# Performance work log

Measured on AMD Instinct MI355X. Metric: run time of the kernel, lower is better.

The kernel has to match this reference:

```python
import jax, jax.numpy as jnp
import numpy as np
import math

DIM = 2048
N_HEADS = 32
N_KV_HEADS = 8
HEAD_DIM = DIM // N_HEADS  # 64
N_REP = N_HEADS // N_KV_HEADS  # 4
BATCH = 1
SEQ = 2048


def rope_cos_sin(seq_len, head_dim, dtype=jnp.float32):
    inv_freq = 1.0 / (10000.0 ** (jnp.arange(0, head_dim, 2, dtype=jnp.float32) / head_dim))
    t = jnp.arange(seq_len, dtype=jnp.float32)
    freqs = jnp.outer(t, inv_freq)            # [S, D/2]
    emb = jnp.concatenate([freqs, freqs], -1)  # [S, D]
    return jnp.cos(emb).astype(dtype), jnp.sin(emb).astype(dtype)


def rotate_half(x):
    x1 = x[..., ::2]
    x2 = x[..., 1::2]
    return jnp.concatenate([-x2, x1], axis=-1)


def setup_inputs() -> dict:
    key = jax.random.key(0)
    ks = jax.random.split(key, 5)
    scale = 1.0 / math.sqrt(DIM)
    x = jax.random.normal(ks[0], (BATCH, SEQ, DIM), jnp.float32)
    wq = jax.random.normal(ks[1], (DIM, N_HEADS * HEAD_DIM), jnp.float32) * scale
    wk = jax.random.normal(ks[2], (DIM, N_KV_HEADS * HEAD_DIM), jnp.float32) * scale
    wv = jax.random.normal(ks[3], (DIM, N_KV_HEADS * HEAD_DIM), jnp.float32) * scale
    wo = jax.random.normal(ks[4], (N_HEADS * HEAD_DIM, DIM), jnp.float32) * scale
    mask = jnp.tril(jnp.ones((SEQ, SEQ), jnp.int32))[None, None]  # [1,1,S,S]
    return {"x": x, "mask": mask, "wq": wq, "wk": wk, "wv": wv, "wo": wo}


def reference(x, mask, wq, wk, wv, wo):
    B, S, _ = x.shape
    q = (x @ wq).reshape(B, S, N_HEADS, HEAD_DIM).transpose(0, 2, 1, 3)     # [B,H,S,D]
    k = (x @ wk).reshape(B, S, N_KV_HEADS, HEAD_DIM).transpose(0, 2, 1, 3)  # [B,Hkv,S,D]
    v = (x @ wv).reshape(B, S, N_KV_HEADS, HEAD_DIM).transpose(0, 2, 1, 3)
    cos, sin = rope_cos_sin(S, HEAD_DIM)  # [S,D]
    q = q * cos + rotate_half(q) * sin
    k = k * cos + rotate_half(k) * sin
    if N_REP > 1:
        k = jnp.repeat(k, N_REP, axis=1)
        v = jnp.repeat(v, N_REP, axis=1)
    scores = jnp.einsum("bhqd,bhkd->bhqk", q, k) / math.sqrt(HEAD_DIM)
    scores = jnp.where(mask == 0, -jnp.inf, scores)
    attn = jax.nn.softmax(scores, axis=-1)
    out = jnp.einsum("bhqk,bhkd->bhqd", attn, v)  # [B,H,S,D]
    out = out.transpose(0, 2, 1, 3).reshape(B, S, N_HEADS * HEAD_DIM)
    return out @ wo
```

## Files before the change

kernel.cpp:

```cpp
#include <hip/hip_runtime.h>
#include <hip/hip_bf16.h>

#define DIM 2048
#define SEQ 2048
#define NH 32
#define HD 64
#define NKV 8
#define QKV_LD 3072

typedef __attribute__((ext_vector_type(8))) short bf16x8;
typedef __attribute__((ext_vector_type(4))) float f32x4;
typedef unsigned short ushort_t;

__device__ inline unsigned short f2bf(float f) {
    union { float f; unsigned int u; } v; v.f = f;
    unsigned int r = v.u + 0x7fffu + ((v.u >> 16) & 1u);
    return (unsigned short)(r >> 16);
}
__device__ inline float bf2f(ushort_t u) {
    union { unsigned int u; float f; } v; v.u = ((unsigned int)u) << 16; return v.f;
}

__device__ inline void async_cp16(const void* g, void* l) {
    __builtin_amdgcn_global_load_lds(
        (const __attribute__((address_space(1))) unsigned int*)g,
        (__attribute__((address_space(3))) unsigned int*)l, 16, 0, 0);
}
__device__ inline void lgkm_fence() {
    __asm__ volatile("s_waitcnt lgkmcnt(0)" ::: "memory");
}

__global__ __launch_bounds__(256) void convert_kernel(
    const float* __restrict__ X, ushort_t* __restrict__ Xb)
{
    int i = (blockIdx.x * 256 + threadIdx.x) * 4;
    float4 v = *(const float4*)(X + i);
    ushort_t o[4] = { f2bf(v.x), f2bf(v.y), f2bf(v.z), f2bf(v.w) };
    *(uint2*)(Xb + i) = *(uint2*)o;
}

__global__ __launch_bounds__(256) void transpose_kernel(
    const float* __restrict__ W, ushort_t* __restrict__ WT, int N)
{
    __shared__ __align__(16) ushort_t tile[64][72];
    const int n0 = blockIdx.x * 64, k0 = blockIdx.y * 64;
    const int t = threadIdx.x;
    {
        const int tk = t >> 4;
        const int tn = (t & 15) * 4;
        #pragma unroll
        for (int i = 0; i < 4; i++) {
            const int k = tk + i * 16;
            float4 v = *(const float4*)(W + (size_t)(k0 + k) * N + n0 + tn);
            tile[tn + 0][k] = f2bf(v.x);
            tile[tn + 1][k] = f2bf(v.y);
            tile[tn + 2][k] = f2bf(v.z);
            tile[tn + 3][k] = f2bf(v.w);
        }
    }
    __syncthreads();
    {
        const int tn = t >> 2;
        const int tk = (t & 3) * 16;
        uint4 a = *(const uint4*)&tile[tn][tk];
        uint4 b = *(const uint4*)&tile[tn][tk + 8];
        ushort_t* dst = WT + (size_t)(n0 + tn) * DIM + k0 + tk;
        *(uint4*)dst = a;
        *(uint4*)(dst + 8) = b;
    }
}

template<int OUT_F32>
__global__ __launch_bounds__(256) void gemm_kernel(
    const ushort_t* __restrict__ A, const ushort_t* __restrict__ BT,
    void* __restrict__ Cout, int K, int lda, int ldo)
{
    __shared__ __align__(16) ushort_t sA[128 * 32];
    __shared__ __align__(16) ushort_t sB[128 * 32];
    const int tn = blockIdx.x * 128, tm = blockIdx.y * 128;
    const int t = threadIdx.x, wave = t >> 6, lane = t & 63;
    const int m16 = lane & 15, quad = lane >> 4;
    const int wr = (wave >> 1) * 64, wc = (wave & 1) * 64;
    const int srow = lane >> 2;
    const int sce = (lane & 3) * 8;

    f32x4 acc[4][4] = {};

    for (int k0 = 0; k0 < K; k0 += 32) {
        __syncthreads();
        #pragma unroll
        for (int p = 0; p < 2; p++) {
            const int j = wave * 2 + p;
            const int row = j * 16 + srow;
            async_cp16(A  + (size_t)(tm + row) * lda + k0 + sce, &sA[j * 512]);
            async_cp16(BT + (size_t)(tn + row) * K   + k0 + sce, &sB[j * 512]);
        }
        __syncthreads();
        bf16x8 af[4], bf[4];
        #pragma unroll
        for (int mt = 0; mt < 4; mt++)
            af[mt] = *(const bf16x8*)&sA[(wr + mt * 16 + m16) * 32 + quad * 8];
        #pragma unroll
        for (int nt = 0; nt < 4; nt++)
            bf[nt] = *(const bf16x8*)&sB[(wc + nt * 16 + m16) * 32 + quad * 8];
        #pragma unroll
        for (int mt = 0; mt < 4; mt++)
            #pragma unroll
            for (int nt = 0; nt < 4; nt++)
                acc[mt][nt] = __builtin_amdgcn_mfma_f32_16x16x32_bf16(af[mt], bf[nt], acc[mt][nt], 0, 0, 0);
    }

    #pragma unroll
    for (int mt = 0; mt < 4; mt++) {
        const int row = tm + wr + mt * 16 + quad * 4;
        #pragma unroll
        for (int nt = 0; nt < 4; nt++) {
            const int col = tn + wc + nt * 16 + m16;
            #pragma unroll
            for (int r = 0; r < 4; r++) {
                if (OUT_F32)
                    ((float*)Cout)[(size_t)(row + r) * ldo + col] = acc[mt][nt][r];
                else
                    ((ushort_t*)Cout)[(size_t)(row + r) * ldo + col] = f2bf(acc[mt][nt][r]);
            }
        }
    }
}

__global__ __launch_bounds__(256) void rope_kernel(ushort_t* qkv, ushort_t* __restrict__ Kr)
{
    const int gid = blockIdx.x * 256 + threadIdx.x;
    const int lane = gid & 63;
    const int idx = gid >> 6;
    const int s = idx / 40;
    const int hh = idx - s * 40;

    const ushort_t* src;
    ushort_t* dst;
    if (hh < 32) {
        dst = qkv + (size_t)s * QKV_LD + hh * 64;
        src = dst;
    } else {
        src = qkv + (size_t)s * QKV_LD + 2048 + (hh - 32) * 64;
        dst = Kr + ((size_t)(hh - 32) * SEQ + s) * 64;
    }

    const float e = bf2f(src[lane]);
    const int i = lane & 31;
    const float freq = __expf(-(float)i * 0.28782313662425572f);
    const float ang = (float)s * freq;
    const float cv = cosf(ang), sv = sinf(ang);
    const int partner = (lane < 32) ? (2 * lane + 1) : (2 * (lane - 32));
    const float y = __shfl(e, partner, 64);
    const float out = (lane < 32) ? (e * cv - y * sv) : (e * cv + y * sv);
    dst[lane] = f2bf(out);
}

__global__ __launch_bounds__(256) void vtrans_kernel(
    const ushort_t* __restrict__ qkv, ushort_t* __restrict__ Vt)
{
    __shared__ __align__(16) ushort_t tile[64][72];
    const int kvh = blockIdx.x & 7;
    const int s0 = (blockIdx.x >> 3) * 64;
    const int t = threadIdx.x;
    {
        const int sr = t >> 3;
        const int d8 = (t & 7) * 8;
        #pragma unroll
        for (int i = 0; i < 2; i++) {
            const int s = sr + i * 32;
            ushort_t tmp[8];
            *(uint4*)tmp = *(const uint4*)(qkv + (size_t)(s0 + s) * QKV_LD + 2560 + kvh * 64 + d8);
            #pragma unroll
            for (int j = 0; j < 8; j++) tile[d8 + j][s] = tmp[j];
        }
    }
    __syncthreads();
    {
        const int dr = t >> 3;
        const int s8 = (t & 7) * 8;
        #pragma unroll
        for (int i = 0; i < 2; i++) {
            const int d = dr + i * 32;
            *(uint4*)(Vt + ((size_t)kvh * 64 + d) * SEQ + s0 + s8) = *(const uint4*)&tile[d][s8];
        }
    }
}

#define SPS 80
__global__ __launch_bounds__(512, 2) void attn_kernel(
    ushort_t* qkv, const ushort_t* __restrict__ Kr, const ushort_t* __restrict__ Vt)
{
    __shared__ __align__(16) ushort_t sP[8][2][16 * SPS];

    const int t = threadIdx.x, wave = t >> 6, lane = t & 63;
    const int m16 = lane & 15, quad = lane >> 4;
    const int h = blockIdx.x & 31;
    const int p = blockIdx.x >> 5;
    const int grp = wave >> 2;
    const int w4 = wave & 3;
    const int band = grp ? p : 15 - p;
    const int kvh = h >> 2;

    const ushort_t* Krh = Kr + (size_t)kvh * SEQ * 64;
    const ushort_t* Vth = Vt + (size_t)kvh * 64 * SEQ;

    const int nkt = band * 2 + 2;

    int qi[2];
    bf16x8 qf[2][2];
    #pragma unroll
    for (int qa = 0; qa < 2; qa++) {
        qi[qa] = band * 128 + (w4 + qa * 4) * 16 + m16;
        const ushort_t* qp = qkv + (size_t)qi[qa] * QKV_LD + h * 64 + quad * 8;
        qf[qa][0] = *(const bf16x8*)qp;
        qf[qa][1] = *(const bf16x8*)(qp + 32);
    }

    f32x4 oacc[2][4] = {};
    float m_run[2] = { -1e30f, -1e30f };
    float l_run[2] = { 0.f, 0.f };

    bf16x8 kf[4][2];
    #pragma unroll
    for (int knt = 0; knt < 4; knt++) {
        const ushort_t* kp = Krh + (size_t)(knt * 16 + m16) * 64 + quad * 8;
        kf[knt][0] = *(const bf16x8*)kp;
        kf[knt][1] = *(const bf16x8*)(kp + 32);
    }

    for (int kt = 0; kt < nkt; kt++) {
        const int kbase = kt * 64;
        const bool last = (kt == nkt - 1);

        f32x4 sc[2][4] = {};
        #pragma unroll
        for (int qa = 0; qa < 2; qa++) {
            if (qa == 0 && last) continue;
            #pragma unroll
            for (int knt = 0; knt < 4; knt++) {
                sc[qa][knt] = __builtin_amdgcn_mfma_f32_16x16x32_bf16(kf[knt][0], qf[qa][0], sc[qa][knt], 0, 0, 0);
                sc[qa][knt] = __builtin_amdgcn_mfma_f32_16x16x32_bf16(kf[knt][1], qf[qa][1], sc[qa][knt], 0, 0, 0);
            }
        }

        bf16x8 vf[4][2];
        #pragma unroll
        for (int nt = 0; nt < 4; nt++) {
            const ushort_t* vp = Vth + (size_t)(nt * 16 + m16) * SEQ + kbase + quad * 8;
            vf[nt][0] = *(const bf16x8*)vp;
            vf[nt][1] = *(const bf16x8*)(vp + 32);
        }
        if (!last) {
            #pragma unroll
            for (int knt = 0; knt < 4; knt++) {
                const ushort_t* kp = Krh + (size_t)(kbase + 64 + knt * 16 + m16) * 64 + quad * 8;
                kf[knt][0] = *(const bf16x8*)kp;
                kf[knt][1] = *(const bf16x8*)(kp + 32);
            }
        }

        #pragma unroll
        for (int qa = 0; qa < 2; qa++) {
            if (qa == 0 && last) continue;
            const bool domask = (qa == 0) ? (kt == nkt - 2) : last;

            float s[16];
            #pragma unroll
            for (int knt = 0; knt < 4; knt++)
                #pragma unroll
                for (int r = 0; r < 4; r++) {
                    float v = sc[qa][knt][r] * 0.125f;
                    if (domask && (kbase + knt * 16 + quad * 4 + r > qi[qa])) v = -1e30f;
                    s[knt * 4 + r] = v;
                }

            float x0 = fmaxf(s[0], s[1]),  x1 = fmaxf(s[2], s[3]);
            float x2 = fmaxf(s[4], s[5]),  x3 = fmaxf(s[6], s[7]);
            float x4 = fmaxf(s[8], s[9]),  x5 = fmaxf(s[10], s[11]);
            float x6 = fmaxf(s[12], s[13]), x7 = fmaxf(s[14], s[15]);
            float rmax = fmaxf(fmaxf(fmaxf(x0, x1), fmaxf(x2, x3)),
                               fmaxf(fmaxf(x4, x5), fmaxf(x6, x7)));
            rmax = fmaxf(rmax, __shfl_xor(rmax, 16, 64));
            rmax = fmaxf(rmax, __shfl_xor(rmax, 32, 64));

            const float mnew = fmaxf(m_run[qa], rmax);
            const float alpha = __expf(m_run[qa] - mnew);
            m_run[qa] = mnew;

            #pragma unroll
            for (int i = 0; i < 16; i++) s[i] = __expf(s[i] - mnew);
            float y0 = s[0] + s[1],  y1 = s[2] + s[3];
            float y2 = s[4] + s[5],  y3 = s[6] + s[7];
            float y4 = s[8] + s[9],  y5 = s[10] + s[11];
            float y6 = s[12] + s[13], y7 = s[14] + s[15];
            float ps = ((y0 + y1) + (y2 + y3)) + ((y4 + y5) + (y6 + y7));
            ps += __shfl_xor(ps, 16, 64);
            ps += __shfl_xor(ps, 32, 64);
            l_run[qa] = l_run[qa] * alpha + ps;

            ushort_t* sPw = sP[wave][qa];
            #pragma unroll
            for (int knt = 0; knt < 4; knt++) {
                unsigned int u0 = (unsigned int)f2bf(s[knt * 4 + 0]) | ((unsigned int)f2bf(s[knt * 4 + 1]) << 16);
                unsigned int u1 = (unsigned int)f2bf(s[knt * 4 + 2]) | ((unsigned int)f2bf(s[knt * 4 + 3]) << 16);
                uint2 pk; pk.x = u0; pk.y = u1;
                *(uint2*)&sPw[m16 * SPS + knt * 16 + quad * 4] = pk;
            }
            lgkm_fence();
            bf16x8 pf0 = *(const bf16x8*)&sPw[m16 * SPS + quad * 8];
            bf16x8 pf1 = *(const bf16x8*)&sPw[m16 * SPS + 32 + quad * 8];

            #pragma unroll
            for (int nt = 0; nt < 4; nt++) {
                #pragma unroll
                for (int r = 0; r < 4; r++) oacc[qa][nt][r] *= alpha;
                oacc[qa][nt] = __builtin_amdgcn_mfma_f32_16x16x32_bf16(vf[nt][0], pf0, oacc[qa][nt], 0, 0, 0);
                oacc[qa][nt] = __builtin_amdgcn_mfma_f32_16x16x32_bf16(vf[nt][1], pf1, oacc[qa][nt], 0, 0, 0);
            }
        }
    }

    #pragma unroll
    for (int qa = 0; qa < 2; qa++) {
        const float rl = 1.f / l_run[qa];
        #pragma unroll
        for (int nt = 0; nt < 4; nt++) {
            ushort_t pk[4];
            #pragma unroll
            for (int r = 0; r < 4; r++) pk[r] = f2bf(oacc[qa][nt][r] * rl);
            *(uint2*)&qkv[(size_t)qi[qa] * QKV_LD + h * 64 + nt * 16 + quad * 4] = *(uint2*)pk;
        }
    }
}

extern "C" void kernel_launch(void* const* d_in, const int* in_sizes, int n_in,
                              void* d_out, int out_size, void* d_ws, size_t ws_size,
                              hipStream_t stream)
{
    const float* x  = (const float*)d_in[0];
    const float* wq = (const float*)d_in[2];
    const float* wk = (const float*)d_in[3];
    const float* wv = (const float*)d_in[4];
    const float* wo = (const float*)d_in[5];

    ushort_t* WT  = (ushort_t*)d_ws;
    ushort_t* xb  = WT + (size_t)3072 * 2048;
    ushort_t* woT = xb;
    ushort_t* qkv = xb + (size_t)2048 * 2048;
    ushort_t* Kr  = qkv + (size_t)SEQ * QKV_LD;
    ushort_t* Vt  = Kr + (size_t)NKV * SEQ * HD;

    dim3 blk(256);

    convert_kernel<<<(DIM * SEQ) / 1024, blk, 0, stream>>>(x, xb);
    transpose_kernel<<<dim3(32, 32), blk, 0, stream>>>(wq, WT, 2048);
    transpose_kernel<<<dim3(8, 32),  blk, 0, stream>>>(wk, WT + (size_t)2048 * 2048, 512);
    transpose_kernel<<<dim3(8, 32),  blk, 0, stream>>>(wv, WT + (size_t)2560 * 2048, 512);

    gemm_kernel<0><<<dim3(QKV_LD / 128, SEQ / 128), blk, 0, stream>>>(xb, WT, qkv, DIM, DIM, QKV_LD);

    transpose_kernel<<<dim3(32, 32), blk, 0, stream>>>(wo, woT, 2048);

    rope_kernel<<<(SEQ * 40 * 64) / 256, blk, 0, stream>>>(qkv, Kr);
    vtrans_kernel<<<NKV * (SEQ / 64), blk, 0, stream>>>(qkv, Vt);

    attn_kernel<<<8 * NH, dim3(512), 0, stream>>>(qkv, Kr, Vt);

    gemm_kernel<1><<<dim3(DIM / 128, SEQ / 128), blk, 0, stream>>>(qkv, woT, d_out, DIM, QKV_LD, DIM);
}
```

Before: 301.5 us.

## Register-only P transpose via permlane swaps, exp2 softmax with lazy rescale

Folds the softmax scale and log2(e) into Q during RoPE so attention can use exp2 directly. The running max is now updated only when the new max exceeds the old one by more than 8, which skips most rescales of the output accumulator. The LDS round trip for P is replaced by packed bf16 conversion plus permlane16/32 swaps that build the MFMA operand in registers, and wave reductions use permlane swaps instead of shuffles. Setprio hints are wrapped around the MFMA blocks. The lazy rescale lets unnormalised values reach up to 2^8, a small precision risk.

Result: no change. 300.4 us (-0.4%).

```diff
diff --git a/kernel.cpp b/kernel.cpp
--- a/kernel.cpp
+++ b/kernel.cpp
@@ -10,6 +10,7 @@
 
 typedef __attribute__((ext_vector_type(8))) short bf16x8;
 typedef __attribute__((ext_vector_type(4))) float f32x4;
+typedef __attribute__((ext_vector_type(2))) unsigned int uint2v;
 typedef unsigned short ushort_t;
 
 __device__ inline unsigned short f2bf(float f) {
@@ -26,8 +27,35 @@
         (const __attribute__((address_space(1))) unsigned int*)g,
         (__attribute__((address_space(3))) unsigned int*)l, 16, 0, 0);
 }
-__device__ inline void lgkm_fence() {
-    __asm__ volatile("s_waitcnt lgkmcnt(0)" ::: "memory");
+
+__device__ inline void pswap32(unsigned int& a, unsigned int& b) {
+    uint2v r = __builtin_amdgcn_permlane32_swap(a, b, false, false);
+    a = r[0]; b = r[1];
+}
+__device__ inline void pswap16(unsigned int& a, unsigned int& b) {
+    uint2v r = __builtin_amdgcn_permlane16_swap(a, b, false, false);
+    a = r[0]; b = r[1];
+}
+__device__ inline float wave_max(float x) {
+    unsigned int a = __float_as_uint(x), b = a;
+    uint2v r = __builtin_amdgcn_permlane16_swap(a, b, false, false);
+    x = fmaxf(__uint_as_float(r[0]), __uint_as_float(r[1]));
+    a = __float_as_uint(x); b = a;
+    r = __builtin_amdgcn_permlane32_swap(a, b, false, false);
+    return fmaxf(__uint_as_float(r[0]), __uint_as_float(r[1]));
+}
+__device__ inline float wave_sum(float x) {
+    unsigned int a = __float_as_uint(x), b = a;
+    uint2v r = __builtin_amdgcn_permlane16_swap(a, b, false, false);
+    x = __uint_as_float(r[0]) + __uint_as_float(r[1]);
+    a = __float_as_uint(x); b = a;
+    r = __builtin_amdgcn_permlane32_swap(a, b, false, false);
+    return __uint_as_float(r[0]) + __uint_as_float(r[1]);
+}
+__device__ inline unsigned int cvt_pk_bf16(float lo, float hi) {
+    unsigned int r;
+    asm volatile("v_cvt_pk_bf16_f32 %0, %1, %2" : "=v"(r) : "v"(lo), "v"(hi));
+    return r;
 }
 
 __global__ __launch_bounds__(256) void convert_kernel(
@@ -127,6 +155,7 @@
     }
 }
 
+#define QSCALE 0.18033688011112042f
 __global__ __launch_bounds__(256) void rope_kernel(ushort_t* qkv, ushort_t* __restrict__ Kr)
 {
     const int gid = blockIdx.x * 256 + threadIdx.x;
@@ -137,7 +166,8 @@
 
     const ushort_t* src;
     ushort_t* dst;
-    if (hh < 32) {
+    const bool isq = (hh < 32);
+    if (isq) {
         dst = qkv + (size_t)s * QKV_LD + hh * 64;
         src = dst;
     } else {
@@ -152,7 +182,8 @@
     const float cv = cosf(ang), sv = sinf(ang);
     const int partner = (lane < 32) ? (2 * lane + 1) : (2 * (lane - 32));
     const float y = __shfl(e, partner, 64);
-    const float out = (lane < 32) ? (e * cv - y * sv) : (e * cv + y * sv);
+    float out = (lane < 32) ? (e * cv - y * sv) : (e * cv + y * sv);
+    if (isq) out *= QSCALE;
     dst[lane] = f2bf(out);
 }
 
@@ -187,12 +218,9 @@
     }
 }
 
-#define SPS 80
 __global__ __launch_bounds__(512, 2) void attn_kernel(
     ushort_t* qkv, const ushort_t* __restrict__ Kr, const ushort_t* __restrict__ Vt)
 {
-    __shared__ __align__(16) ushort_t sP[8][2][16 * SPS];
-
     const int t = threadIdx.x, wave = t >> 6, lane = t & 63;
     const int m16 = lane & 15, quad = lane >> 4;
     const int h = blockIdx.x & 31;
@@ -234,6 +262,7 @@
         const bool last = (kt == nkt - 1);
 
         f32x4 sc[2][4] = {};
+        __builtin_amdgcn_s_setprio(1);
         #pragma unroll
         for (int qa = 0; qa < 2; qa++) {
             if (qa == 0 && last) continue;
@@ -243,6 +272,7 @@
                 sc[qa][knt] = __builtin_amdgcn_mfma_f32_16x16x32_bf16(kf[knt][1], qf[qa][1], sc[qa][knt], 0, 0, 0);
             }
         }
+        __builtin_amdgcn_s_setprio(0);
 
         bf16x8 vf[4][2];
         #pragma unroll
@@ -270,7 +300,7 @@
             for (int knt = 0; knt < 4; knt++)
                 #pragma unroll
                 for (int r = 0; r < 4; r++) {
-                    float v = sc[qa][knt][r] * 0.125f;
+                    float v = sc[qa][knt][r];
                     if (domask && (kbase + knt * 16 + quad * 4 + r > qi[qa])) v = -1e30f;
                     s[knt * 4 + r] = v;
                 }
@@ -281,43 +311,48 @@
             float x6 = fmaxf(s[12], s[13]), x7 = fmaxf(s[14], s[15]);
             float rmax = fmaxf(fmaxf(fmaxf(x0, x1), fmaxf(x2, x3)),
                                fmaxf(fmaxf(x4, x5), fmaxf(x6, x7)));
-            rmax = fmaxf(rmax, __shfl_xor(rmax, 16, 64));
-            rmax = fmaxf(rmax, __shfl_xor(rmax, 32, 64));
-
-            const float mnew = fmaxf(m_run[qa], rmax);
-            const float alpha = __expf(m_run[qa] - mnew);
-            m_run[qa] = mnew;
-
-            #pragma unroll
-            for (int i = 0; i < 16; i++) s[i] = __expf(s[i] - mnew);
+            rmax = wave_max(rmax);
+
+            if (rmax > m_run[qa] + 8.f) {
+                const float mnew = fmaxf(m_run[qa], rmax);
+                const float alpha = __builtin_amdgcn_exp2f(m_run[qa] - mnew);
+                m_run[qa] = mnew;
+                l_run[qa] *= alpha;
+                #pragma unroll
+                for (int nt = 0; nt < 4; nt++)
+                    #pragma unroll
+                    for (int r = 0; r < 4; r++) oacc[qa][nt][r] *= alpha;
+            }
+            const float m = m_run[qa];
+
+            #pragma unroll
+            for (int i = 0; i < 16; i++) s[i] = __builtin_amdgcn_exp2f(s[i] - m);
             float y0 = s[0] + s[1],  y1 = s[2] + s[3];
             float y2 = s[4] + s[5],  y3 = s[6] + s[7];
             float y4 = s[8] + s[9],  y5 = s[10] + s[11];
             float y6 = s[12] + s[13], y7 = s[14] + s[15];
             float ps = ((y0 + y1) + (y2 + y3)) + ((y4 + y5) + (y6 + y7));
-            ps += __shfl_xor(ps, 16, 64);
-            ps += __shfl_xor(ps, 32, 64);
-            l_run[qa] = l_run[qa] * alpha + ps;
-
-            ushort_t* sPw = sP[wave][qa];
-            #pragma unroll
-            for (int knt = 0; knt < 4; knt++) {
-                unsigned int u0 = (unsigned int)f2bf(s[knt * 4 + 0]) | ((unsigned int)f2bf(s[knt * 4 + 1]) << 16);
-                unsigned int u1 = (unsigned int)f2bf(s[knt * 4 + 2]) | ((unsigned int)f2bf(s[knt * 4 + 3]) << 16);
-                uint2 pk; pk.x = u0; pk.y = u1;
-                *(uint2*)&sPw[m16 * SPS + knt * 16 + quad * 4] = pk;
+            l_run[qa] += wave_sum(ps);
+
+            unsigned int u00 = cvt_pk_bf16(s[0],  s[1]),  u01 = cvt_pk_bf16(s[2],  s[3]);
+            unsigned int u10 = cvt_pk_bf16(s[4],  s[5]),  u11 = cvt_pk_bf16(s[6],  s[7]);
+            unsigned int u20 = cvt_pk_bf16(s[8],  s[9]),  u21 = cvt_pk_bf16(s[10], s[11]);
+            unsigned int u30 = cvt_pk_bf16(s[12], s[13]), u31 = cvt_pk_bf16(s[14], s[15]);
+            pswap32(u00, u10); pswap16(u00, u10);
+            pswap32(u01, u11); pswap16(u01, u11);
+            pswap32(u20, u30); pswap16(u20, u30);
+            pswap32(u21, u31); pswap16(u21, u31);
+            union { unsigned int w[4]; bf16x8 v; } P0, P1;
+            P0.w[0] = u00; P0.w[1] = u01; P0.w[2] = u10; P0.w[3] = u11;
+            P1.w[0] = u20; P1.w[1] = u21; P1.w[2] = u30; P1.w[3] = u31;
+
+            __builtin_amdgcn_s_setprio(1);
+            #pragma unroll
+            for (int nt = 0; nt < 4; nt++) {
+                oacc[qa][nt] = __builtin_amdgcn_mfma_f32_16x16x32_bf16(vf[nt][0], P0.v, oacc[qa][nt], 0, 0, 0);
+                oacc[qa][nt] = __builtin_amdgcn_mfma_f32_16x16x32_bf16(vf[nt][1], P1.v, oacc[qa][nt], 0, 0, 0);
             }
-            lgkm_fence();
-            bf16x8 pf0 = *(const bf16x8*)&sPw[m16 * SPS + quad * 8];
-            bf16x8 pf1 = *(const bf16x8*)&sPw[m16 * SPS + 32 + quad * 8];
-
-            #pragma unroll
-            for (int nt = 0; nt < 4; nt++) {
-                #pragma unroll
-                for (int r = 0; r < 4; r++) oacc[qa][nt][r] *= alpha;
-                oacc[qa][nt] = __builtin_amdgcn_mfma_f32_16x16x32_bf16(vf[nt][0], pf0, oacc[qa][nt], 0, 0, 0);
-                oacc[qa][nt] = __builtin_amdgcn_mfma_f32_16x16x32_bf16(vf[nt][1], pf1, oacc[qa][nt], 0, 0, 0);
-            }
+            __builtin_amdgcn_s_setprio(0);
         }
     }
 
```
